# Kernel tuning notes

Measured on AMD Instinct MI355X. Metric: run time of the kernel, lower is better.

The kernel has to match this reference:

```python
import jax, jax.numpy as jnp
import numpy as np

NUM_THINGS = 80
NUM_STUFF = 53
IGNORE_CLASS = NUM_THINGS + NUM_STUFF  # 133, default ignore_class == -1 path
OVERLAP_THR = 0.5
STUFF_AREA_THR = 4096
THING_CONF_THR = 0.5
INSTANCE_OFFSET = 1000
NUM_SEM_CLASSES = NUM_THINGS + NUM_STUFF + 1  # label range [0, 133]


def setup_inputs() -> dict:
    key = jax.random.key(0)
    k1, k2, k3, k4 = jax.random.split(key, 4)
    B, N, H, W = 2, 100, 800, 1344
    ins_masks = jax.random.randint(k1, (B, N, H, W), 0, 2).astype(jnp.bool_)
    ins_scores = jax.random.uniform(k2, (B, N), dtype=jnp.float32)
    ins_class_ids = jax.random.randint(k3, (B, N), 0, NUM_THINGS, dtype=jnp.int32)
    sem_masks = jax.random.randint(k4, (B, H, W), 0, NUM_SEM_CLASSES, dtype=jnp.int32)
    return {"ins_masks": ins_masks, "ins_scores": ins_scores,
            "ins_class_ids": ins_class_ids, "sem_masks": sem_masks}


def _combine_segms(masks, scores, cls_ids, sem):
    # masks: [N,H,W] bool, scores: [N] f32, cls_ids: [N] i32, sem: [H,W] i32
    order = jnp.argsort(-scores)  # descending by score
    masks = masks[order]
    scores = scores[order]
    cls_ids = cls_ids[order]

    def step(carry, xs):
        pan, iid = carry  # pan: [H,W] i32, iid: i32 (next instance id)
        m, s, c = xs
        area = jnp.sum(m).astype(jnp.float32)
        inter = jnp.sum(m & (pan != 0)).astype(jnp.float32)
        keep = (s >= THING_CONF_THR) & (area > 0) & (inter <= OVERLAP_THR * area)
        write = keep & m & (pan == 0)  # only overwrite free pixels
        pan = jnp.where(write, c + iid * INSTANCE_OFFSET, pan)
        iid = iid + keep.astype(jnp.int32)
        return (pan, iid), None

    pan0 = jnp.zeros(masks.shape[1:], dtype=jnp.int32)
    (pan, _), _ = jax.lax.scan(step, (pan0, jnp.int32(1)), (masks, scores, cls_ids))

    # Stuff fusion: pixels claimed by things become ignore class, then any
    # remaining semantic class with area >= thr (and not ignored) is written.
    sem2 = jnp.where(pan > 0, IGNORE_CLASS, sem)
    counts = jnp.zeros((NUM_SEM_CLASSES,), jnp.int32).at[sem2.ravel()].add(1)
    valid = counts >= STUFF_AREA_THR
    valid = valid.at[IGNORE_CLASS].set(False)
    pan = jnp.where(valid[sem2], sem2 + NUM_THINGS, pan)
    return pan


def reference(ins_masks, ins_scores, ins_class_ids, sem_masks):
    # Batched greedy panoptic fusion -> [B,H,W] int32
    return jax.vmap(_combine_segms)(ins_masks, ins_scores, ins_class_ids, sem_masks)
```

## Files before the change

kernel.cpp:

```cpp
#include <hip/hip_runtime.h>
#include <stdint.h>

#define NB 2
#define NN 100
#define HWP (800*1344)
#define G 10
#define NCH 7
#define NKEY (1<<(G+1))
#define CBIT (1u<<G)
#define NSEM 134
#define IGN 133
#define THR 1024
#define BPI 128
#define GRID (NB*BPI)
#define PPB (HWP/BPI)
#define GPX 8
#define NG (PPB/GPX)
#define MCAP 64

struct WS {
  unsigned hist[NCH][NB][NKEY];
  unsigned counts[NB][NSEM];
  int      iid[NB][NN];
  unsigned kmaskArr[NCH][NB];
  unsigned kcAfter[NCH][NB];
  int      order[NB][NN];
  float    score_s[NB][NN];
  int      cls_s[NB][NN];
  unsigned Mcnt[NB];
  unsigned flag;
};
#define ZW (NCH*NB*NKEY + NB*NSEM + NB*NN + NCH*NB*2)

__device__ __forceinline__ unsigned u8x8_to_bits(uint2 v) {
  unsigned lo = (((v.x & 0x01010101u) * 0x01020408u) >> 24) & 0xFu;
  unsigned hi = (((v.y & 0x01010101u) * 0x01020408u) >> 24) & 0xFu;
  return lo | (hi << 4);
}

__device__ __forceinline__ unsigned load8(const void* __restrict__ masks,
                                          size_t eo, int mode_u8) {
  if (mode_u8) return u8x8_to_bits(*(const uint2*)((const uint8_t*)masks + eo));
  const uint4* mp = (const uint4*)((const int*)masks + eo);
  uint4 a = mp[0], b = mp[1];
  return (a.x & 1u) | ((a.y & 1u) << 1) | ((a.z & 1u) << 2) | ((a.w & 1u) << 3) |
         ((b.x & 1u) << 4) | ((b.y & 1u) << 5) | ((b.z & 1u) << 6) | ((b.w & 1u) << 7);
}

__global__ __launch_bounds__(THR) void k0_setup(
    const void* __restrict__ masks, const float* __restrict__ scores,
    const int* __restrict__ cls, WS* __restrict__ ws) {
  const int t = threadIdx.x, gid = blockIdx.x;
  unsigned* zp = &ws->hist[0][0][0];
  for (unsigned i = (unsigned)gid * THR + t; i < (unsigned)ZW; i += (unsigned)GRID * THR)
    zp[i] = 0;
  if (gid == 0) {
    __shared__ float ss[NB * NN];
    __shared__ unsigned shDet;
    const unsigned* mw = (const unsigned*)masks;
    unsigned any = 0;
    for (int i = t; i < 4096; i += THR) any |= (mw[i] > 1u) ? 1u : 0u;
    if (t == 0) shDet = 0;
    if (t < NB * NN) ss[t] = scores[t];
    if (t < NB) ws->Mcnt[t] = 0;
    __syncthreads();
    if (any) atomicOr(&shDet, 1u);
    __syncthreads();
    if (t == 0) ws->flag = shDet;
    if (t < NB * NN) {
      int bb = t / NN, i = t % NN;
      float s = ss[bb * NN + i];
      if (s >= 0.5f) {
        int r = 0;
        for (int j = 0; j < NN; ++j) {
          float sj = ss[bb * NN + j];
          if (sj >= 0.5f && (sj > s || (sj == s && j < i))) r++;
        }
        ws->order[bb][r]   = i;
        ws->score_s[bb][r] = s;
        ws->cls_s[bb][r]   = cls[bb * NN + i];
        atomicAdd(&ws->Mcnt[bb], 1u);
      }
    }
  }
}

__global__ __launch_bounds__(THR, 4) void k_passA(
    const void* __restrict__ masks, WS* __restrict__ ws,
    unsigned long long* __restrict__ w1) {
  __shared__ unsigned lh[NKEY];
  __shared__ int midx[MCAP];
  const int t = threadIdx.x, gid = blockIdx.x;
  const int b = gid / BPI, bx = gid % BPI;
  int M = (int)ws->Mcnt[b]; if (M > MCAP) M = MCAP;
  for (int i = t; i < NKEY; i += THR) lh[i] = 0;
  if (t < MCAP) midx[t] = ws->order[b][t < M ? t : 0];
  __syncthreads();
  const int mode_u8 = (int)ws->flag;
  const size_t sb = (size_t)bx * PPB;
  for (int s = 0; s < 2; ++s) {
    int gr = s * THR + t;
    if (gr >= NG) break;
    const int l0 = gr * GPX;
    const size_t off = sb + l0;
    unsigned long long w[GPX];
    #pragma unroll
    for (int k = 0; k < GPX; ++k) w[k] = 0;
    for (int g0 = 0; g0 < M; g0 += 8) {
      int n = M - g0; if (n > 8) n = 8;
      int mi[8];
      #pragma unroll
      for (int u = 0; u < 8; ++u)
        mi[u] = __builtin_amdgcn_readfirstlane(midx[g0 + (u < n ? u : 0)]);
      #pragma unroll
      for (int u = 0; u < 8; ++u) {
        if (u < n) {
          unsigned b8 = load8(masks, (size_t)(b * NN + mi[u]) * HWP + off, mode_u8);
          #pragma unroll
          for (int k = 0; k < GPX; ++k)
            w[k] |= (unsigned long long)((b8 >> k) & 1u) << (g0 + u);
        }
      }
    }
    unsigned long long* wp = w1 + (size_t)b * HWP + off;
    #pragma unroll
    for (int k = 0; k < GPX; ++k) wp[k] = w[k];
    #pragma unroll
    for (int k = 0; k < GPX; ++k)
      atomicAdd(&lh[(unsigned)(w[k] & (unsigned long long)(CBIT - 1u))], 1u);
  }
  __syncthreads();
  for (int i = t; i < NKEY; i += THR) {
    unsigned v = lh[i];
    if (v) atomicAdd(&ws->hist[0][b][i], v);
  }
}

__global__ __launch_bounds__(THR, 4) void k_chunk(
    const int* __restrict__ sem, WS* __restrict__ ws,
    const unsigned long long* __restrict__ w1, int c, int doCounts) {
  __shared__ unsigned lh[NKEY];
  __shared__ unsigned sh_kmask;
  const int t = threadIdx.x, gid = blockIdx.x;
  const int b = gid / BPI, bx = gid % BPI;
  int M = (int)ws->Mcnt[b]; if (M > MCAP) M = MCAP;
  int Lp = M - (c - 1) * G; if (Lp > G) Lp = G;
  int Lc = (c < NCH) ? (M - c * G) : 0; if (Lc > G) Lc = G;
  if (Lc < 0) Lc = 0;
  if (!doCounts && Lp <= 0 && Lc <= 0) return;

  unsigned h[32];
  if (Lp > 0) {
    for (int i = t; i < NKEY; i += THR) lh[i] = ws->hist[c - 1][b][i];
    __syncthreads();
    if (t < 64) {
      #pragma unroll
      for (int j = 0; j < 32; ++j) h[j] = lh[t + (j << 6)];
    }
    __syncthreads();
  }
  if (Lc > 0) { for (int i = t; i < NKEY; i += THR) lh[i] = 0; }
  else if (doCounts) { for (int i = t; i < NSEM; i += THR) lh[i] = 0; }
  if (Lp > 0) {
    if (t < 64) {
      unsigned km = 0;
      unsigned kc = (c >= 2) ? ws->kcAfter[c - 2][b] : 0u;
      for (int g = 0; g < Lp; ++g) {
        unsigned sel = km & ((1u << g) - 1u);
        unsigned area = 0, inter = 0;
        #pragma unroll
        for (int j = 0; j < 32; ++j) {
          unsigned i = (unsigned)t + ((unsigned)j << 6);
          if ((i >> g) & 1u) {
            area += h[j];
            if ((i >> G) | (i & sel)) inter += h[j];
          }
        }
        #pragma unroll
        for (int off = 32; off; off >>= 1) {
          area  += __shfl_xor(area, off);
          inter += __shfl_xor(inter, off);
        }
        float s = ws->score_s[b][(c - 1) * G + g];
        bool keep = (s >= 0.5f) && (area > 0u) && (2u * inter <= area);
        if (keep) {
          km |= 1u << g; kc += 1u;
          if (t == 0 && bx == 0) ws->iid[b][(c - 1) * G + g] = (int)kc;
        }
      }
      if (t == 0) {
        sh_kmask = km;
        ws->kmaskArr[c - 1][b] = km;
        if (bx == 0) ws->kcAfter[c - 1][b] = kc;
      }
    }
  } else if (t == 0) sh_kmask = 0;
  __syncthreads();

  if (Lc <= 0 && !doCounts) return;

  unsigned long long keptPrev =
      (unsigned long long)sh_kmask << ((c - 1) * G);
  for (int j = 0; j < c - 1; ++j)
    keptPrev |= (unsigned long long)ws->kmaskArr[j][b] << (j * G);

  const size_t base = (size_t)b * HWP + (size_t)bx * PPB;
  const int sh = (c < NCH) ? c * G : 0;
  for (int s = 0; s < 2; ++s) {
    int gr = s * THR + t;
    if (gr >= NG) break;
    const int l0 = gr * GPX;
    const unsigned long long* wp = w1 + base + l0;
    unsigned long long w[GPX];
    #pragma unroll
    for (int k = 0; k < GPX; ++k) w[k] = wp[k];
    if (Lc > 0) {
      #pragma unroll
      for (int k = 0; k < GPX; ++k) {
        unsigned key = (unsigned)((w[k] >> sh) & (unsigned long long)(CBIT - 1u));
        if (w[k] & keptPrev) key |= CBIT;
        atomicAdd(&lh[key], 1u);
      }
    }
    if (doCounts) {
      const uint4* sp = (const uint4*)(sem + base + l0);
      uint4 sv0 = sp[0], sv1 = sp[1];
      unsigned sarr[8] = {sv0.x, sv0.y, sv0.z, sv0.w, sv1.x, sv1.y, sv1.z, sv1.w};
      #pragma unroll
      for (int k = 0; k < GPX; ++k)
        if (!(w[k] & keptPrev) && sarr[k] != (unsigned)IGN)
          atomicAdd(&lh[sarr[k]], 1u);
    }
  }
  __syncthreads();
  if (Lc > 0) {
    for (int i = t; i < NKEY; i += THR) {
      unsigned v = lh[i];
      if (v) atomicAdd(&ws->hist[c][b][i], v);
    }
  } else if (doCounts) {
    for (int i = t; i < NSEM; i += THR) {
      unsigned v = lh[i];
      if (v) atomicAdd(&ws->counts[b][i], v);
    }
  }
}

__global__ __launch_bounds__(THR) void k_writepan(
    const int* __restrict__ sem, const unsigned long long* __restrict__ w1,
    const WS* __restrict__ ws, int* __restrict__ out) {
  __shared__ int pval[NN];
  __shared__ int sval[NSEM];
  const int t = threadIdx.x, gid = blockIdx.x;
  const int b = gid / BPI, bx = gid % BPI;
  const size_t base = (size_t)b * HWP + (size_t)bx * PPB;
  if (t < NN)  pval[t] = ws->cls_s[b][t] + ws->iid[b][t] * 1000;
  if (t < NSEM) sval[t] = (t != IGN && ws->counts[b][t] >= 4096u) ? (t + 80) : 0;
  __syncthreads();
  unsigned long long keptAll = 0;
  #pragma unroll
  for (int j = 0; j < NCH; ++j)
    keptAll |= (unsigned long long)ws->kmaskArr[j][b] << (j * G);
  for (int s = 0; s < 2; ++s) {
    int gr = s * THR + t;
    if (gr >= NG) break;
    const int l0 = gr * GPX;
    const unsigned long long* wp = w1 + base + l0;
    unsigned long long w[GPX];
    #pragma unroll
    for (int k = 0; k < GPX; ++k) w[k] = wp[k];
    const uint4* sp = (const uint4*)(sem + base + l0);
    uint4 sv0 = sp[0], sv1 = sp[1];
    unsigned sarr[8] = {sv0.x, sv0.y, sv0.z, sv0.w, sv1.x, sv1.y, sv1.z, sv1.w};
    int4* op = (int4*)(out + base + l0);
    #pragma unroll
    for (int q = 0; q < 2; ++q) {
      int res[4];
      #pragma unroll
      for (int j = 0; j < 4; ++j) {
        int k = q * 4 + j;
        unsigned long long hit = w[k] & keptAll;
        res[j] = hit ? pval[__builtin_ctzll(hit)] : sval[sarr[k]];
      }
      op[q] = make_int4(res[0], res[1], res[2], res[3]);
    }
  }
}

extern "C" void kernel_launch(void* const* d_in, const int* in_sizes, int n_in,
                              void* d_out, int out_size, void* d_ws, size_t ws_size,
                              hipStream_t stream) {
  const void*  masks  = d_in[0];
  const float* scores = (const float*)d_in[1];
  const int*   cls    = (const int*)d_in[2];
  const int*   sem    = (const int*)d_in[3];
  int* out = (int*)d_out;

  uint8_t* base = (uint8_t*)d_ws;
  WS* ws = (WS*)base;
  size_t off = (sizeof(WS) + 255) & ~(size_t)255;
  unsigned long long* w1 = (unsigned long long*)(base + off);

  hipLaunchKernelGGL(k0_setup, dim3(GRID), dim3(THR), 0, stream,
                     masks, scores, cls, ws);
  hipLaunchKernelGGL(k_passA, dim3(GRID), dim3(THR), 0, stream, masks, ws, w1);
  for (int c = 1; c < NCH; ++c)
    hipLaunchKernelGGL(k_chunk, dim3(GRID), dim3(THR), 0, stream,
                       sem, ws, w1, c, 0);
  hipLaunchKernelGGL(k_chunk, dim3(GRID), dim3(THR), 0, stream,
                     sem, ws, w1, NCH, 1);
  hipLaunchKernelGGL(k_writepan, dim3(GRID), dim3(THR), 0, stream,
                     sem, w1, ws, out);
}
```

Before: 201.8 us.

## Store masks as per-instance bitplanes and track claimed pixels in a bitmap

Pass A now builds per-instance 1-bit planes with wave ballots (one 64-bit word per 64 pixels per instance) instead of a 64-bit per-pixel word array. The chunk kernels read only the current chunk's planes plus a claimed-pixel byte bitmap, and update that bitmap from the planes of newly kept instances. The final write kernel walks the kept instance planes in rank order to find the first hit per pixel. This is meant to cut intermediate memory traffic from 8 bytes per pixel to 1 bit per instance, at the cost of more, smaller byte loads and a serial loop over kept instances in the write pass.

```diff
diff --git a/kernel.cpp b/kernel.cpp
--- a/kernel.cpp
+++ b/kernel.cpp
@@ -4,19 +4,21 @@
 #define NB 2
 #define NN 100
 #define HWP (800*1344)
-#define G 10
+#define GCH 10
 #define NCH 7
-#define NKEY (1<<(G+1))
-#define CBIT (1u<<G)
+#define NKEY (1<<(GCH+1))
+#define CBIT (1u<<GCH)
 #define NSEM 134
 #define IGN 133
 #define THR 1024
 #define BPI 128
 #define GRID (NB*BPI)
 #define PPB (HWP/BPI)
-#define GPX 8
-#define NG (PPB/GPX)
+#define NG (PPB/8)
 #define MCAP 64
+#define NWRD (HWP/64)
+#define NBYT (HWP/8)
+#define WPI (BPI*16)
 
 struct WS {
   unsigned hist[NCH][NB][NKEY];
@@ -32,28 +34,15 @@
 };
 #define ZW (NCH*NB*NKEY + NB*NSEM + NB*NN + NCH*NB*2)
 
-__device__ __forceinline__ unsigned u8x8_to_bits(uint2 v) {
-  unsigned lo = (((v.x & 0x01010101u) * 0x01020408u) >> 24) & 0xFu;
-  unsigned hi = (((v.y & 0x01010101u) * 0x01020408u) >> 24) & 0xFu;
-  return lo | (hi << 4);
-}
-
-__device__ __forceinline__ unsigned load8(const void* __restrict__ masks,
-                                          size_t eo, int mode_u8) {
-  if (mode_u8) return u8x8_to_bits(*(const uint2*)((const uint8_t*)masks + eo));
-  const uint4* mp = (const uint4*)((const int*)masks + eo);
-  uint4 a = mp[0], b = mp[1];
-  return (a.x & 1u) | ((a.y & 1u) << 1) | ((a.z & 1u) << 2) | ((a.w & 1u) << 3) |
-         ((b.x & 1u) << 4) | ((b.y & 1u) << 5) | ((b.z & 1u) << 6) | ((b.w & 1u) << 7);
-}
-
 __global__ __launch_bounds__(THR) void k0_setup(
     const void* __restrict__ masks, const float* __restrict__ scores,
-    const int* __restrict__ cls, WS* __restrict__ ws) {
+    const int* __restrict__ cls, WS* __restrict__ ws, unsigned* __restrict__ clmW) {
   const int t = threadIdx.x, gid = blockIdx.x;
+  unsigned tg = (unsigned)gid * THR + t;
   unsigned* zp = &ws->hist[0][0][0];
-  for (unsigned i = (unsigned)gid * THR + t; i < (unsigned)ZW; i += (unsigned)GRID * THR)
-    zp[i] = 0;
+  if (tg < (unsigned)ZW) zp[tg] = 0;
+  const unsigned cw = (unsigned)(NB * NBYT / 4);
+  for (unsigned i = tg; i < cw; i += (unsigned)GRID * THR) clmW[i] = 0;
   if (gid == 0) {
     __shared__ float ss[NB * NN];
     __shared__ unsigned shDet;
@@ -87,7 +76,7 @@
 
 __global__ __launch_bounds__(THR, 4) void k_passA(
     const void* __restrict__ masks, WS* __restrict__ ws,
-    unsigned long long* __restrict__ w1) {
+    unsigned long long* __restrict__ bpW) {
   __shared__ unsigned lh[NKEY];
   __shared__ int midx[MCAP];
   const int t = threadIdx.x, gid = blockIdx.x;
@@ -96,38 +85,35 @@
   for (int i = t; i < NKEY; i += THR) lh[i] = 0;
   if (t < MCAP) midx[t] = ws->order[b][t < M ? t : 0];
   __syncthreads();
-  const int mode_u8 = (int)ws->flag;
-  const size_t sb = (size_t)bx * PPB;
-  for (int s = 0; s < 2; ++s) {
-    int gr = s * THR + t;
-    if (gr >= NG) break;
-    const int l0 = gr * GPX;
-    const size_t off = sb + l0;
-    unsigned long long w[GPX];
-    #pragma unroll
-    for (int k = 0; k < GPX; ++k) w[k] = 0;
-    for (int g0 = 0; g0 < M; g0 += 8) {
-      int n = M - g0; if (n > 8) n = 8;
-      int mi[8];
-      #pragma unroll
-      for (int u = 0; u < 8; ++u)
-        mi[u] = __builtin_amdgcn_readfirstlane(midx[g0 + (u < n ? u : 0)]);
-      #pragma unroll
-      for (int u = 0; u < 8; ++u) {
-        if (u < n) {
-          unsigned b8 = load8(masks, (size_t)(b * NN + mi[u]) * HWP + off, mode_u8);
-          #pragma unroll
-          for (int k = 0; k < GPX; ++k)
-            w[k] |= (unsigned long long)((b8 >> k) & 1u) << (g0 + u);
-        }
-      }
-    }
-    unsigned long long* wp = w1 + (size_t)b * HWP + off;
-    #pragma unroll
-    for (int k = 0; k < GPX; ++k) wp[k] = w[k];
-    #pragma unroll
-    for (int k = 0; k < GPX; ++k)
-      atomicAdd(&lh[(unsigned)(w[k] & (unsigned long long)(CBIT - 1u))], 1u);
+  if (M > 0) {
+    const int mode_u8 = (int)ws->flag;
+    const int wv = t >> 6, lane = t & 63;
+    const uint8_t* m8 = (const uint8_t*)masks;
+    const int*     m32 = (const int*)masks;
+    for (int w = bx * 16 + wv; w < NWRD; w += WPI) {
+      const size_t p = (size_t)w * 64 + lane;
+      unsigned key = 0;
+      for (int r0 = 0; r0 < M; r0 += 8) {
+        int n = M - r0; if (n > 8) n = 8;
+        unsigned vals[8];
+        #pragma unroll
+        for (int u = 0; u < 8; ++u) {
+          int r = r0 + (u < n ? u : 0);
+          int mi = __builtin_amdgcn_readfirstlane(midx[r]);
+          size_t eo = (size_t)(b * NN + mi) * HWP + p;
+          vals[u] = mode_u8 ? (unsigned)m8[eo] : (unsigned)m32[eo];
+        }
+        #pragma unroll
+        for (int u = 0; u < 8; ++u) {
+          if (u < n) {
+            unsigned long long bm = __ballot(vals[u] & 1u);
+            if (lane == 0) bpW[(size_t)(b * MCAP + r0 + u) * NWRD + w] = bm;
+            if (r0 + u < GCH) key |= (vals[u] & 1u) << (r0 + u);
+          }
+        }
+      }
+      atomicAdd(&lh[key], 1u);
+    }
   }
   __syncthreads();
   for (int i = t; i < NKEY; i += THR) {
@@ -138,31 +124,24 @@
 
 __global__ __launch_bounds__(THR, 4) void k_chunk(
     const int* __restrict__ sem, WS* __restrict__ ws,
-    const unsigned long long* __restrict__ w1, int c, int doCounts) {
+    const uint8_t* __restrict__ bpB, uint8_t* __restrict__ clm,
+    int c, int doCounts) {
   __shared__ unsigned lh[NKEY];
   __shared__ unsigned sh_kmask;
   const int t = threadIdx.x, gid = blockIdx.x;
   const int b = gid / BPI, bx = gid % BPI;
   int M = (int)ws->Mcnt[b]; if (M > MCAP) M = MCAP;
-  int Lp = M - (c - 1) * G; if (Lp > G) Lp = G;
-  int Lc = (c < NCH) ? (M - c * G) : 0; if (Lc > G) Lc = G;
+  int Lp = M - (c - 1) * GCH; if (Lp > GCH) Lp = GCH;
+  int Lc = (c < NCH) ? (M - c * GCH) : 0; if (Lc > GCH) Lc = GCH;
   if (Lc < 0) Lc = 0;
-  if (!doCounts && Lp <= 0 && Lc <= 0) return;
-
-  unsigned h[32];
-  if (Lp > 0) {
-    for (int i = t; i < NKEY; i += THR) lh[i] = ws->hist[c - 1][b][i];
-    __syncthreads();
-    if (t < 64) {
-      #pragma unroll
-      for (int j = 0; j < 32; ++j) h[j] = lh[t + (j << 6)];
-    }
-    __syncthreads();
-  }
-  if (Lc > 0) { for (int i = t; i < NKEY; i += THR) lh[i] = 0; }
-  else if (doCounts) { for (int i = t; i < NSEM; i += THR) lh[i] = 0; }
+  if (!doCounts && Lp <= 0) return;
+
   if (Lp > 0) {
     if (t < 64) {
+      const unsigned* __restrict__ hp = &ws->hist[c - 1][b][0];
+      unsigned h[32];
+      #pragma unroll
+      for (int j = 0; j < 32; ++j) h[j] = hp[t + (j << 6)];
       unsigned km = 0;
       unsigned kc = (c >= 2) ? ws->kcAfter[c - 2][b] : 0u;
       for (int g = 0; g < Lp; ++g) {
@@ -173,7 +152,7 @@
           unsigned i = (unsigned)t + ((unsigned)j << 6);
           if ((i >> g) & 1u) {
             area += h[j];
-            if ((i >> G) | (i & sel)) inter += h[j];
+            if ((i >> GCH) | (i & sel)) inter += h[j];
           }
         }
         #pragma unroll
@@ -181,11 +160,11 @@
           area  += __shfl_xor(area, off);
           inter += __shfl_xor(inter, off);
         }
-        float s = ws->score_s[b][(c - 1) * G + g];
+        float s = ws->score_s[b][(c - 1) * GCH + g];
         bool keep = (s >= 0.5f) && (area > 0u) && (2u * inter <= area);
         if (keep) {
           km |= 1u << g; kc += 1u;
-          if (t == 0 && bx == 0) ws->iid[b][(c - 1) * G + g] = (int)kc;
+          if (t == 0 && bx == 0) ws->iid[b][(c - 1) * GCH + g] = (int)kc;
         }
       }
       if (t == 0) {
@@ -195,40 +174,50 @@
       }
     }
   } else if (t == 0) sh_kmask = 0;
-  __syncthreads();
-
-  if (Lc <= 0 && !doCounts) return;
-
-  unsigned long long keptPrev =
-      (unsigned long long)sh_kmask << ((c - 1) * G);
-  for (int j = 0; j < c - 1; ++j)
-    keptPrev |= (unsigned long long)ws->kmaskArr[j][b] << (j * G);
-
-  const size_t base = (size_t)b * HWP + (size_t)bx * PPB;
-  const int sh = (c < NCH) ? c * G : 0;
+
+  if (Lc > 0) { for (int i = t; i < NKEY; i += THR) lh[i] = 0; }
+  else if (doCounts) { for (int i = t; i < NSEM; i += THR) lh[i] = 0; }
+  __syncthreads();
+
+  const unsigned kmask = sh_kmask;
+  const uint8_t* prevP = bpB + (size_t)(b * MCAP + (c - 1) * GCH) * NBYT;
+  const uint8_t* curP  = bpB + (size_t)(b * MCAP + (c < NCH ? c * GCH : 0)) * NBYT;
+  uint8_t* clmb = clm + (size_t)b * NBYT;
+
   for (int s = 0; s < 2; ++s) {
     int gr = s * THR + t;
     if (gr >= NG) break;
-    const int l0 = gr * GPX;
-    const unsigned long long* wp = w1 + base + l0;
-    unsigned long long w[GPX];
-    #pragma unroll
-    for (int k = 0; k < GPX; ++k) w[k] = wp[k];
+    const int idx = bx * NG + gr;
+    unsigned cb = clmb[idx];
+    if (kmask) {
+      unsigned rem = kmask, nw = 0;
+      while (rem) {
+        int g = __builtin_ctz(rem); rem &= rem - 1u;
+        nw |= (unsigned)prevP[(size_t)g * NBYT + idx];
+      }
+      unsigned cb2 = cb | nw;
+      if (cb2 != cb) clmb[idx] = (uint8_t)cb2;
+      cb = cb2;
+    }
     if (Lc > 0) {
-      #pragma unroll
-      for (int k = 0; k < GPX; ++k) {
-        unsigned key = (unsigned)((w[k] >> sh) & (unsigned long long)(CBIT - 1u));
-        if (w[k] & keptPrev) key |= CBIT;
-        atomicAdd(&lh[key], 1u);
-      }
+      unsigned key[8];
+      #pragma unroll
+      for (int k = 0; k < 8; ++k) key[k] = ((cb >> k) & 1u) << GCH;
+      for (int g = 0; g < Lc; ++g) {
+        unsigned pb = (unsigned)curP[(size_t)g * NBYT + idx];
+        #pragma unroll
+        for (int k = 0; k < 8; ++k) key[k] |= ((pb >> k) & 1u) << g;
+      }
+      #pragma unroll
+      for (int k = 0; k < 8; ++k) atomicAdd(&lh[key[k]], 1u);
     }
     if (doCounts) {
-      const uint4* sp = (const uint4*)(sem + base + l0);
+      const uint4* sp = (const uint4*)(sem + (size_t)b * HWP + (size_t)idx * 8);
       uint4 sv0 = sp[0], sv1 = sp[1];
       unsigned sarr[8] = {sv0.x, sv0.y, sv0.z, sv0.w, sv1.x, sv1.y, sv1.z, sv1.w};
       #pragma unroll
-      for (int k = 0; k < GPX; ++k)
-        if (!(w[k] & keptPrev) && sarr[k] != (unsigned)IGN)
+      for (int k = 0; k < 8; ++k)
+        if (!((cb >> k) & 1u) && sarr[k] != (unsigned)IGN)
           atomicAdd(&lh[sarr[k]], 1u);
     }
   }
@@ -247,40 +236,57 @@
 }
 
 __global__ __launch_bounds__(THR) void k_writepan(
-    const int* __restrict__ sem, const unsigned long long* __restrict__ w1,
+    const int* __restrict__ sem, const uint8_t* __restrict__ bpB,
     const WS* __restrict__ ws, int* __restrict__ out) {
   __shared__ int pval[NN];
   __shared__ int sval[NSEM];
+  __shared__ uint8_t keptR[MCAP];
+  __shared__ int shK;
   const int t = threadIdx.x, gid = blockIdx.x;
   const int b = gid / BPI, bx = gid % BPI;
-  const size_t base = (size_t)b * HWP + (size_t)bx * PPB;
   if (t < NN)  pval[t] = ws->cls_s[b][t] + ws->iid[b][t] * 1000;
   if (t < NSEM) sval[t] = (t != IGN && ws->counts[b][t] >= 4096u) ? (t + 80) : 0;
-  __syncthreads();
-  unsigned long long keptAll = 0;
-  #pragma unroll
-  for (int j = 0; j < NCH; ++j)
-    keptAll |= (unsigned long long)ws->kmaskArr[j][b] << (j * G);
+  if (t == 0) {
+    int K = 0;
+    for (int j = 0; j < NCH; ++j) {
+      unsigned km = ws->kmaskArr[j][b];
+      while (km) { int g = __builtin_ctz(km); km &= km - 1u;
+                   keptR[K++] = (uint8_t)(j * GCH + g); }
+    }
+    shK = K;
+  }
+  __syncthreads();
+  const int K = shK;
+  const uint8_t* pb0 = bpB + (size_t)(b * MCAP) * NBYT;
   for (int s = 0; s < 2; ++s) {
     int gr = s * THR + t;
     if (gr >= NG) break;
-    const int l0 = gr * GPX;
-    const unsigned long long* wp = w1 + base + l0;
-    unsigned long long w[GPX];
+    const int idx = bx * NG + gr;
+    int orank[8];
     #pragma unroll
-    for (int k = 0; k < GPX; ++k) w[k] = wp[k];
-    const uint4* sp = (const uint4*)(sem + base + l0);
+    for (int k = 0; k < 8; ++k) orank[k] = 0;
+    unsigned rem8 = 0xFFu;
+    for (int i = 0; i < K; ++i) {
+      int r = keptR[i];
+      unsigned hit = (unsigned)pb0[(size_t)r * NBYT + idx] & rem8;
+      if (hit) {
+        #pragma unroll
+        for (int k = 0; k < 8; ++k)
+          if ((hit >> k) & 1u) orank[k] = r;
+        rem8 &= ~hit;
+      }
+    }
+    const uint4* sp = (const uint4*)(sem + (size_t)b * HWP + (size_t)idx * 8);
     uint4 sv0 = sp[0], sv1 = sp[1];
     unsigned sarr[8] = {sv0.x, sv0.y, sv0.z, sv0.w, sv1.x, sv1.y, sv1.z, sv1.w};
-    int4* op = (int4*)(out + base + l0);
+    int4* op = (int4*)(out + (size_t)b * HWP + (size_t)idx * 8);
     #pragma unroll
     for (int q = 0; q < 2; ++q) {
       int res[4];
       #pragma unroll
       for (int j = 0; j < 4; ++j) {
         int k = q * 4 + j;
-        unsigned long long hit = w[k] & keptAll;
-        res[j] = hit ? pval[__builtin_ctzll(hit)] : sval[sarr[k]];
+        res[j] = ((rem8 >> k) & 1u) ? sval[sarr[k]] : pval[orank[k]];
       }
       op[q] = make_int4(res[0], res[1], res[2], res[3]);
     }
@@ -299,16 +305,17 @@
   uint8_t* base = (uint8_t*)d_ws;
   WS* ws = (WS*)base;
   size_t off = (sizeof(WS) + 255) & ~(size_t)255;
-  unsigned long long* w1 = (unsigned long long*)(base + off);
+  unsigned long long* bpW = (unsigned long long*)(base + off);
+  uint8_t* clm = base + off + (size_t)NB * MCAP * NWRD * 8;
 
   hipLaunchKernelGGL(k0_setup, dim3(GRID), dim3(THR), 0, stream,
-                     masks, scores, cls, ws);
-  hipLaunchKernelGGL(k_passA, dim3(GRID), dim3(THR), 0, stream, masks, ws, w1);
+                     masks, scores, cls, ws, (unsigned*)clm);
+  hipLaunchKernelGGL(k_passA, dim3(GRID), dim3(THR), 0, stream, masks, ws, bpW);
   for (int c = 1; c < NCH; ++c)
     hipLaunchKernelGGL(k_chunk, dim3(GRID), dim3(THR), 0, stream,
-                       sem, ws, w1, c, 0);
+                       sem, ws, (const uint8_t*)bpW, clm, c, 0);
   hipLaunchKernelGGL(k_chunk, dim3(GRID), dim3(THR), 0, stream,
-                     sem, ws, w1, NCH, 1);
+                     sem, ws, (const uint8_t*)bpW, clm, NCH, 1);
   hipLaunchKernelGGL(k_writepan, dim3(GRID), dim3(THR), 0, stream,
-                     sem, w1, ws, out);
-}
+                     sem, (const uint8_t*)bpW, ws, out);
+}
```

New measurement: 277.3 us. +37.4%, slower.
